# Kernel tuning notes

Measured on AMD Instinct MI355X. Metric: run time of the kernel, lower is better.

The kernel has to match this reference:

```python
import jax, jax.numpy as jnp
import numpy as np

B, T, D, H, O = 64, 512, 512, 2048, 7

def setup_inputs() -> dict:
    key = jax.random.key(0)
    ks = jax.random.split(key, 12)
    s_ih = 1.0 / np.sqrt(H)
    return {
        "x":    jax.random.normal(ks[0], (B, T, D), dtype=jnp.float32),
        # LSTMCell params (PyTorch gate order i,f,g,o stacked along dim 0)
        "W_ih": jax.random.uniform(ks[1], (4 * H, D), jnp.float32, -s_ih, s_ih),
        "b_ih": jax.random.uniform(ks[2], (4 * H,), jnp.float32, -s_ih, s_ih),
        "W_hh": jax.random.uniform(ks[3], (4 * H, H), jnp.float32, -s_ih, s_ih),
        "b_hh": jax.random.uniform(ks[4], (4 * H,), jnp.float32, -s_ih, s_ih),
        # init_h / init_c Linear(D -> H)
        "W_h0": jax.random.normal(ks[5], (H, D), jnp.float32) * np.sqrt(2.0 / D),
        "b_h0": jnp.zeros((H,), jnp.float32),
        "W_c0": jax.random.normal(ks[6], (H, D), jnp.float32) * np.sqrt(2.0 / D),
        "b_c0": jnp.zeros((H,), jnp.float32),
        # fc Linear(H -> O), kaiming init, zero bias
        "W_fc": jax.random.normal(ks[7], (O, H), jnp.float32) * np.sqrt(2.0 / H),
        "b_fc": jnp.zeros((O,), jnp.float32),
    }

def reference(x, W_ih, b_ih, W_hh, b_hh, W_h0, b_h0, W_c0, b_c0, W_fc, b_fc):
    # init hidden state from mean over time (module's init_hidden_state)
    mean_x = x.mean(axis=1)                       # [B, D]
    h0 = mean_x @ W_h0.T + b_h0                   # [B, H]
    c0 = mean_x @ W_c0.T + b_c0                   # [B, H]

    def step(carry, xt):
        h, c = carry
        gates = xt @ W_ih.T + b_ih + h @ W_hh.T + b_hh   # [B, 4H]
        i, f, g, o = jnp.split(gates, 4, axis=1)
        i = jax.nn.sigmoid(i)
        f = jax.nn.sigmoid(f)
        g = jnp.tanh(g)
        o = jax.nn.sigmoid(o)
        c = f * c + i * g
        h = o * jnp.tanh(c)
        return (h, c), h

    xs = jnp.swapaxes(x, 0, 1)                    # [T, B, D]
    _, hs = jax.lax.scan(step, (h0, c0), xs)      # hs: [T, B, H]
    # dropout(p=0.5) is identity in eval mode; fc per timestep
    poses = jnp.einsum('tbh,oh->bto', hs, W_fc) + b_fc   # [B, T, O]
    return poses
```

## Files before the change

kernel.cpp:

```cpp
#include <hip/hip_runtime.h>
#include <hip/hip_cooperative_groups.h>

namespace cg = cooperative_groups;

#define Bb 64
#define Tt 512
#define Dd 512
#define Hh 2048
#define Oo 7
#define NKT 80
#define NWG 256
#define NTHR 512
#define SP 36
#define HSTEP 131072
#define XSTEP 32768

typedef short bf16x8 __attribute__((ext_vector_type(8)));
typedef float f32x4 __attribute__((ext_vector_type(4)));

__device__ __forceinline__ unsigned short f2bf(float f) {
  unsigned u = __float_as_uint(f);
  return (unsigned short)((u + 0x7FFFu + ((u >> 16) & 1u)) >> 16);
}
__device__ __forceinline__ float bf2f(unsigned short s) {
  return __uint_as_float(((unsigned)s) << 16);
}
__device__ __forceinline__ float sigm(float x) { return 1.0f / (1.0f + __expf(-x)); }
__device__ __forceinline__ float tanh_(float x) {
  x = fminf(15.0f, fmaxf(-15.0f, x));
  float e = __expf(2.0f * x);
  return (e - 1.0f) / (e + 1.0f);
}

__global__ void __launch_bounds__(NTHR, 2) lstm_fused(
    const float* __restrict__ x,
    const float* __restrict__ W_ih, const float* __restrict__ b_ih,
    const float* __restrict__ W_hh, const float* __restrict__ b_hh,
    const float* __restrict__ W_h0, const float* __restrict__ b_h0,
    const float* __restrict__ W_c0, const float* __restrict__ b_c0,
    const float* __restrict__ W_fc, const float* __restrict__ b_fc,
    float* __restrict__ out,
    short* __restrict__ Wbf,
    unsigned short* __restrict__ Hbuf,
    float* __restrict__ cbuf,
    float* __restrict__ meanx,
    float* __restrict__ bsum,
    unsigned short* __restrict__ xbf,
    unsigned* __restrict__ flags)
{
  const int wg = blockIdx.x, tid = threadIdx.x;
  const int gtid = wg * NTHR + tid;
  cg::grid_group grid = cg::this_grid();
  __shared__ float smem[8 * 64 * SP];

  {
    int b = wg >> 2;
    int d = ((wg & 3) << 7) + (tid & 127);
    int th = tid >> 7;
    const float* xp = x + (size_t)b * Tt * Dd + d;
    float s = 0.f;
    for (int t = th * 128; t < th * 128 + 128; ++t) s += xp[(size_t)t * Dd];
    smem[tid] = s;
    __syncthreads();
    if (tid < 128) {
      float tot = smem[tid] + smem[tid + 128] + smem[tid + 256] + smem[tid + 384];
      meanx[b * Dd + ((wg & 3) << 7) + tid] = tot * (1.0f / Tt);
    }
    __syncthreads();
  }

  {
    const int NSLOT = (8192 * 2560) / 8;
    for (int slot = gtid; slot < NSLOT; slot += NWG * NTHR) {
      int lane = slot & 63;
      int fr = slot >> 6;
      int kt = fr % 80;
      int ntw = fr / 80;
      int nl = ((ntw & 1) << 4) + (lane & 15);
      int w = ntw >> 1;
      int row = ((nl >> 3) << 11) + (w << 3) + (nl & 7);
      int kb = (kt << 5) + ((lane >> 4) << 3);
      const float* src = (kb < 512) ? (W_ih + (size_t)row * 512 + kb)
                                    : (W_hh + (size_t)row * 2048 + (kb - 512));
      float4 u0 = *reinterpret_cast<const float4*>(src);
      float4 u1 = *reinterpret_cast<const float4*>(src + 4);
      bf16x8 v;
      v[0] = (short)f2bf(u0.x); v[1] = (short)f2bf(u0.y);
      v[2] = (short)f2bf(u0.z); v[3] = (short)f2bf(u0.w);
      v[4] = (short)f2bf(u1.x); v[5] = (short)f2bf(u1.y);
      v[6] = (short)f2bf(u1.z); v[7] = (short)f2bf(u1.w);
      *reinterpret_cast<bf16x8*>(Wbf + (size_t)slot * 8) = v;
    }
    const int NX = (Bb * Tt * Dd) / 8;
    for (int s = gtid; s < NX; s += NWG * NTHR) {
      int q  = s & 3;
      int b  = (s >> 2) & 63;
      int kt = (s >> 8) & 15;
      int t  = s >> 12;
      const float* p = x + (size_t)b * (Tt * Dd) + (size_t)t * Dd + (kt << 5) + (q << 3);
      float4 u0 = *reinterpret_cast<const float4*>(p);
      float4 u1 = *reinterpret_cast<const float4*>(p + 4);
      bf16x8 v;
      v[0] = (short)f2bf(u0.x); v[1] = (short)f2bf(u0.y);
      v[2] = (short)f2bf(u0.z); v[3] = (short)f2bf(u0.w);
      v[4] = (short)f2bf(u1.x); v[5] = (short)f2bf(u1.y);
      v[6] = (short)f2bf(u1.z); v[7] = (short)f2bf(u1.w);
      *reinterpret_cast<bf16x8*>((short*)xbf + (size_t)s * 8) = v;
    }
    if (gtid < NWG)
      __hip_atomic_store(&flags[gtid], 0u, __ATOMIC_RELAXED, __HIP_MEMORY_SCOPE_AGENT);
    if (gtid < 8192) bsum[gtid] = b_ih[gtid] + b_hh[gtid];
  }
  grid.sync();

  {
    for (int q = tid; q < 1024; q += NTHR) {
      int which = q >> 9;
      int b = (q >> 3) & 63;
      int j = q & 7;
      int n = (wg << 3) + j;
      const float* Wr = (which ? W_c0 : W_h0) + (size_t)n * 512;
      const float* mx = meanx + b * 512;
      float acc0 = which ? b_c0[n] : b_h0[n];
      for (int d = 0; d < 512; ++d) acc0 += mx[d] * Wr[d];
      if (which) cbuf[b * Hh + n] = acc0;
      else       Hbuf[((n >> 5) << 11) + (b << 5) + (n & 31)] = f2bf(acc0);
    }
  }
  grid.sync();

  const int wave = tid >> 6, lane = tid & 63;
  const int ml = lane & 15;
  const int kg = lane >> 4;
  const short* wb0 = Wbf + (size_t)(wg * 2) * NKT * 512;
  const short* wb1 = wb0 + (size_t)NKT * 512;

  bf16x8 w0x[2], w0h[8], w1x[2], w1h[8];
#pragma unroll
  for (int i = 0; i < 2; ++i) {
    int kt = (wave << 1) + i;
    w0x[i] = *reinterpret_cast<const bf16x8*>(wb0 + ((size_t)kt << 9) + (lane << 3));
    w1x[i] = *reinterpret_cast<const bf16x8*>(wb1 + ((size_t)kt << 9) + (lane << 3));
  }
#pragma unroll
  for (int i = 0; i < 8; ++i) {
    int kt = 16 + (wave << 3) + i;
    w0h[i] = *reinterpret_cast<const bf16x8*>(wb0 + ((size_t)kt << 9) + (lane << 3));
    w1h[i] = *reinterpret_cast<const bf16x8*>(wb1 + ((size_t)kt << 9) + (lane << 3));
  }

  const int cb = tid >> 3, cj = tid & 7;
  const int cn = (wg << 3) + cj;
  float cv = cbuf[cb * Hh + cn];
  const float bi = bsum[cn],        bfs = bsum[2048 + cn];
  const float bg = bsum[4096 + cn], bo = bsum[6144 + cn];

  f32x4 acc[4][2];
#pragma unroll
  for (int mt = 0; mt < 4; ++mt) {
    acc[mt][0] = (f32x4){0.f, 0.f, 0.f, 0.f};
    acc[mt][1] = (f32x4){0.f, 0.f, 0.f, 0.f};
  }

  auto xpart = [&](int tx) {
#pragma unroll
    for (int i = 0; i < 2; ++i) {
      int kt = (wave << 1) + i;
      const unsigned short* xb = xbf + (size_t)tx * XSTEP + ((size_t)kt << 11) + (kg << 3);
      bf16x8 afr[4];
#pragma unroll
      for (int mt = 0; mt < 4; ++mt) {
        int m = (mt << 4) + ml;
        afr[mt] = *reinterpret_cast<const bf16x8*>(xb + (m << 5));
      }
#pragma unroll
      for (int mt = 0; mt < 4; ++mt) {
        acc[mt][0] = __builtin_amdgcn_mfma_f32_16x16x32_bf16(afr[mt], w0x[i], acc[mt][0], 0, 0, 0);
        acc[mt][1] = __builtin_amdgcn_mfma_f32_16x16x32_bf16(afr[mt], w1x[i], acc[mt][1], 0, 0, 0);
      }
    }
  };

  auto waitwave = [&](unsigned tw) {
    const unsigned* fl = flags + ((wave << 5) | (lane & 31));
    while (__hip_atomic_load(fl, __ATOMIC_RELAXED, __HIP_MEMORY_SCOPE_AGENT) < tw)
      __builtin_amdgcn_s_sleep(2);
    asm volatile("" ::: "memory");
  };

  auto waitall = [&](unsigned tw) {
    if (wave == 0) {
      const unsigned* fl = flags + (lane << 2);
      for (;;) {
        unsigned m0 = __hip_atomic_load(&fl[0], __ATOMIC_RELAXED, __HIP_MEMORY_SCOPE_AGENT);
        unsigned m1 = __hip_atomic_load(&fl[1], __ATOMIC_RELAXED, __HIP_MEMORY_SCOPE_AGENT);
        unsigned m2 = __hip_atomic_load(&fl[2], __ATOMIC_RELAXED, __HIP_MEMORY_SCOPE_AGENT);
        unsigned m3 = __hip_atomic_load(&fl[3], __ATOMIC_RELAXED, __HIP_MEMORY_SCOPE_AGENT);
        unsigned mn = min(min(m0, m1), min(m2, m3));
        if (__all(mn >= tw)) break;
        __builtin_amdgcn_s_sleep(2);
      }
    }
    asm volatile("" ::: "memory");
    __syncthreads();
  };

  xpart(0);

  for (int t = 1; t <= Tt; ++t) {
    if (t > 1) waitwave((unsigned)(t - 1));
#pragma unroll
    for (int i = 0; i < 8; ++i) {
      int kth = (wave << 3) + i;
      const unsigned short* hb = Hbuf + (size_t)(t - 1) * HSTEP + ((size_t)kth << 11) + (kg << 3);
      bf16x8 afr[4];
#pragma unroll
      for (int mt = 0; mt < 4; ++mt) {
        int m = (mt << 4) + ml;
        afr[mt] = *reinterpret_cast<const bf16x8*>(hb + (m << 5));
      }
#pragma unroll
      for (int mt = 0; mt < 4; ++mt) {
        acc[mt][0] = __builtin_amdgcn_mfma_f32_16x16x32_bf16(afr[mt], w0h[i], acc[mt][0], 0, 0, 0);
        acc[mt][1] = __builtin_amdgcn_mfma_f32_16x16x32_bf16(afr[mt], w1h[i], acc[mt][1], 0, 0, 0);
      }
    }
#pragma unroll
    for (int mt = 0; mt < 4; ++mt) {
      int r0 = (mt << 4) + (kg << 2);
#pragma unroll
      for (int r = 0; r < 4; ++r) {
        smem[((wave << 6) + r0 + r) * SP + ml] = acc[mt][0][r];
        smem[((wave << 6) + r0 + r) * SP + 16 + ml] = acc[mt][1][r];
      }
    }
    __syncthreads();
    unsigned* hout32 = (unsigned*)(Hbuf + (size_t)t * HSTEP);
    {
      float gi = 0.f, gf_ = 0.f, gg = 0.f, go = 0.f;
#pragma unroll
      for (int w2 = 0; w2 < 8; ++w2) {
        const float* sp = &smem[((w2 << 6) + cb) * SP];
        gi += sp[cj];       gf_ += sp[8 + cj];
        gg += sp[16 + cj];  go += sp[24 + cj];
      }
      gi += bi; gf_ += bfs; gg += bg; go += bo;
      cv = sigm(gf_) * cv + sigm(gi) * tanh_(gg);
      float hv = sigm(go) * tanh_(cv);
      float hv_hi = __shfl_down(hv, 1);
      if (!(tid & 1)) {
        unsigned pk = ((unsigned)f2bf(hv_hi) << 16) | (unsigned)f2bf(hv);
        int soff = ((cn >> 5) << 11) + (cb << 5) + (cn & 31);
        __hip_atomic_store(&hout32[soff >> 1], pk,
                           __ATOMIC_RELAXED, __HIP_MEMORY_SCOPE_AGENT);
      }
    }
    asm volatile("s_waitcnt vmcnt(0)" ::: "memory");
    __syncthreads();
    if (tid == 0)
      __hip_atomic_store(&flags[wg], (unsigned)t,
                         __ATOMIC_RELAXED, __HIP_MEMORY_SCOPE_AGENT);
#pragma unroll
    for (int mt = 0; mt < 4; ++mt) {
      acc[mt][0] = (f32x4){0.f, 0.f, 0.f, 0.f};
      acc[mt][1] = (f32x4){0.f, 0.f, 0.f, 0.f};
    }
    if (t < Tt) xpart(t);
  }

  waitall((unsigned)Tt);

  for (int i = tid; i < Oo * Hh; i += NTHR) smem[i] = W_fc[i];
  __syncthreads();
  if (gtid < Bb * Tt) {
    int b = gtid & 63, tq = gtid >> 6;
    const unsigned short* hrw = Hbuf + (size_t)(tq + 1) * HSTEP + (b << 5);
    float acco[7];
#pragma unroll
    for (int o = 0; o < 7; ++o) acco[o] = b_fc[o];
    for (int k = 0; k < Hh; k += 8) {
      bf16x8 hv = *reinterpret_cast<const bf16x8*>(hrw + ((k >> 5) << 11) + (k & 31));
      float hf[8];
#pragma unroll
      for (int e = 0; e < 8; ++e) hf[e] = bf2f((unsigned short)hv[e]);
#pragma unroll
      for (int o = 0; o < 7; ++o) {
        const float* wr = &smem[o * Hh + k];
        float s = 0.f;
#pragma unroll
        for (int e = 0; e < 8; ++e) s += hf[e] * wr[e];
        acco[o] += s;
      }
    }
    float* op = out + ((size_t)b * Tt + tq) * Oo;
#pragma unroll
    for (int o = 0; o < 7; ++o) op[o] = acco[o];
  }
}

extern "C" void kernel_launch(void* const* d_in, const int* in_sizes, int n_in,
                              void* d_out, int out_size, void* d_ws, size_t ws_size,
                              hipStream_t stream) {
  (void)in_sizes; (void)n_in;
  const float* x    = (const float*)d_in[0];
  const float* W_ih = (const float*)d_in[1];
  const float* b_ih = (const float*)d_in[2];
  const float* W_hh = (const float*)d_in[3];
  const float* b_hh = (const float*)d_in[4];
  const float* W_h0 = (const float*)d_in[5];
  const float* b_h0 = (const float*)d_in[6];
  const float* W_c0 = (const float*)d_in[7];
  const float* b_c0 = (const float*)d_in[8];
  const float* W_fc = (const float*)d_in[9];
  const float* b_fc = (const float*)d_in[10];
  float* out = (float*)d_out;

  char* ws = (char*)d_ws;
  size_t off = 0;
  short* Wbf = (short*)(ws + off);            off += (size_t)8192 * 2560 * 2;
  unsigned short* Hbuf = (unsigned short*)(ws + off); off += (size_t)513 * 64 * 2048 * 2;
  float* cbuf = (float*)(ws + off);           off += (size_t)64 * 2048 * 4;
  float* meanx = (float*)(ws + off);          off += (size_t)64 * 512 * 4;
  float* bsum = (float*)(ws + off);           off += (size_t)8192 * 4;
  unsigned short* xbf = (unsigned short*)(ws + off); off += (size_t)64 * 512 * 512 * 2;
  unsigned* flags = (unsigned*)(ws + off);    off += (size_t)NWG * 4;

  if (ws_size < off) {
    hipMemsetAsync(d_out, 0, (size_t)out_size * 4, stream);
    return;
  }

  void* args[] = {&x, &W_ih, &b_ih, &W_hh, &b_hh, &W_h0, &b_h0, &W_c0, &b_c0,
                  &W_fc, &b_fc, &out, &Wbf, &Hbuf, &cbuf, &meanx, &bsum, &xbf, &flags};
  hipLaunchCooperativeKernel((void*)lstm_fused, dim3(NWG), dim3(NTHR), args, 0, stream);
}
```

Measured before the change: 3.925 ms.

## Split batch across workgroup halves and stream weights from global per step

Repartitions the persistent LSTM so each workgroup owns 32 batch rows and 16 hidden units (64 gate columns) instead of all 64 rows and 8 hidden units. Waits now depend only on the 128 workgroups in the same batch half, which shrinks the set of producers each step has to wait for. Weights are no longer kept in registers and are reloaded from global memory (L2) every timestep, raising per-step load traffic. The reduction buffer layout and the h packing shuffle are adjusted to match.

```diff
diff --git a/kernel.cpp b/kernel.cpp
--- a/kernel.cpp
+++ b/kernel.cpp
@@ -11,9 +11,10 @@
 #define NKT 80
 #define NWG 256
 #define NTHR 512
-#define SP 36
+#define SP 70
 #define HSTEP 131072
 #define XSTEP 32768
+#define WSLC (NKT * 512)
 
 typedef short bf16x8 __attribute__((ext_vector_type(8)));
 typedef float f32x4 __attribute__((ext_vector_type(4)));
@@ -51,7 +52,9 @@
   const int wg = blockIdx.x, tid = threadIdx.x;
   const int gtid = wg * NTHR + tid;
   cg::grid_group grid = cg::this_grid();
-  __shared__ float smem[8 * 64 * SP];
+  __shared__ float smem[256 * SP];
+
+  const int bh = wg >> 7, cgp = wg & 127;
 
   {
     int b = wg >> 2;
@@ -114,17 +117,18 @@
   grid.sync();
 
   {
-    for (int q = tid; q < 1024; q += NTHR) {
-      int which = q >> 9;
-      int b = (q >> 3) & 63;
-      int j = q & 7;
-      int n = (wg << 3) + j;
+    for (int q2 = tid; q2 < 1024; q2 += NTHR) {
+      int which = q2 >> 9;
+      int r = q2 & 511;
+      int lb2 = r >> 4, j = r & 15;
+      int b = (bh << 5) + lb2;
+      int n = (cgp << 4) + j;
       const float* Wr = (which ? W_c0 : W_h0) + (size_t)n * 512;
       const float* mx = meanx + b * 512;
-      float acc0 = which ? b_c0[n] : b_h0[n];
-      for (int d = 0; d < 512; ++d) acc0 += mx[d] * Wr[d];
-      if (which) cbuf[b * Hh + n] = acc0;
-      else       Hbuf[((n >> 5) << 11) + (b << 5) + (n & 31)] = f2bf(acc0);
+      float a0 = which ? b_c0[n] : b_h0[n];
+      for (int d = 0; d < 512; ++d) a0 += mx[d] * Wr[d];
+      if (which) cbuf[b * Hh + n] = a0;
+      else       Hbuf[((n >> 5) << 11) + (b << 5) + (n & 31)] = f2bf(a0);
     }
   }
   grid.sync();
@@ -132,57 +136,44 @@
   const int wave = tid >> 6, lane = tid & 63;
   const int ml = lane & 15;
   const int kg = lane >> 4;
-  const short* wb0 = Wbf + (size_t)(wg * 2) * NKT * 512;
-  const short* wb1 = wb0 + (size_t)NKT * 512;
-
-  bf16x8 w0x[2], w0h[8], w1x[2], w1h[8];
-#pragma unroll
-  for (int i = 0; i < 2; ++i) {
-    int kt = (wave << 1) + i;
-    w0x[i] = *reinterpret_cast<const bf16x8*>(wb0 + ((size_t)kt << 9) + (lane << 3));
-    w1x[i] = *reinterpret_cast<const bf16x8*>(wb1 + ((size_t)kt << 9) + (lane << 3));
-  }
-#pragma unroll
-  for (int i = 0; i < 8; ++i) {
-    int kt = 16 + (wave << 3) + i;
-    w0h[i] = *reinterpret_cast<const bf16x8*>(wb0 + ((size_t)kt << 9) + (lane << 3));
-    w1h[i] = *reinterpret_cast<const bf16x8*>(wb1 + ((size_t)kt << 9) + (lane << 3));
-  }
-
-  const int cb = tid >> 3, cj = tid & 7;
-  const int cn = (wg << 3) + cj;
-  float cv = cbuf[cb * Hh + cn];
+  const short* wbase = Wbf + (size_t)(cgp << 2) * WSLC;
+
+  const int lb = tid & 31, hc = tid >> 5;
+  const int cbn = (bh << 5) + lb;
+  const int cn  = (cgp << 4) + hc;
+  float cv = cbuf[cbn * Hh + cn];
   const float bi = bsum[cn],        bfs = bsum[2048 + cn];
   const float bg = bsum[4096 + cn], bo = bsum[6144 + cn];
 
-  f32x4 acc[4][2];
-#pragma unroll
-  for (int mt = 0; mt < 4; ++mt) {
-    acc[mt][0] = (f32x4){0.f, 0.f, 0.f, 0.f};
-    acc[mt][1] = (f32x4){0.f, 0.f, 0.f, 0.f};
-  }
+  f32x4 acc[2][4];
+#pragma unroll
+  for (int mt = 0; mt < 2; ++mt)
+#pragma unroll
+    for (int q = 0; q < 4; ++q) acc[mt][q] = (f32x4){0.f, 0.f, 0.f, 0.f};
 
   auto xpart = [&](int tx) {
 #pragma unroll
     for (int i = 0; i < 2; ++i) {
       int kt = (wave << 1) + i;
-      const unsigned short* xb = xbf + (size_t)tx * XSTEP + ((size_t)kt << 11) + (kg << 3);
-      bf16x8 afr[4];
-#pragma unroll
-      for (int mt = 0; mt < 4; ++mt) {
-        int m = (mt << 4) + ml;
-        afr[mt] = *reinterpret_cast<const bf16x8*>(xb + (m << 5));
-      }
-#pragma unroll
-      for (int mt = 0; mt < 4; ++mt) {
-        acc[mt][0] = __builtin_amdgcn_mfma_f32_16x16x32_bf16(afr[mt], w0x[i], acc[mt][0], 0, 0, 0);
-        acc[mt][1] = __builtin_amdgcn_mfma_f32_16x16x32_bf16(afr[mt], w1x[i], acc[mt][1], 0, 0, 0);
+      const unsigned short* xb = xbf + (size_t)tx * XSTEP + ((size_t)kt << 11)
+                                     + (bh << 10) + (kg << 3);
+      bf16x8 afr[2];
+#pragma unroll
+      for (int mt = 0; mt < 2; ++mt)
+        afr[mt] = *reinterpret_cast<const bf16x8*>(xb + (((mt << 4) + ml) << 5));
+      const short* wk = wbase + ((size_t)kt << 9) + (lane << 3);
+#pragma unroll
+      for (int q = 0; q < 4; ++q) {
+        bf16x8 bq = *reinterpret_cast<const bf16x8*>(wk + (size_t)q * WSLC);
+#pragma unroll
+        for (int mt = 0; mt < 2; ++mt)
+          acc[mt][q] = __builtin_amdgcn_mfma_f32_16x16x32_bf16(afr[mt], bq, acc[mt][q], 0, 0, 0);
       }
     }
   };
 
   auto waitwave = [&](unsigned tw) {
-    const unsigned* fl = flags + ((wave << 5) | (lane & 31));
+    const unsigned* fl = flags + (bh << 7) + (wave << 4) + (lane & 15);
     while (__hip_atomic_load(fl, __ATOMIC_RELAXED, __HIP_MEMORY_SCOPE_AGENT) < tw)
       __builtin_amdgcn_s_sleep(2);
     asm volatile("" ::: "memory");
@@ -211,27 +202,30 @@
     if (t > 1) waitwave((unsigned)(t - 1));
 #pragma unroll
     for (int i = 0; i < 8; ++i) {
-      int kth = (wave << 3) + i;
-      const unsigned short* hb = Hbuf + (size_t)(t - 1) * HSTEP + ((size_t)kth << 11) + (kg << 3);
-      bf16x8 afr[4];
-#pragma unroll
-      for (int mt = 0; mt < 4; ++mt) {
-        int m = (mt << 4) + ml;
-        afr[mt] = *reinterpret_cast<const bf16x8*>(hb + (m << 5));
-      }
-#pragma unroll
-      for (int mt = 0; mt < 4; ++mt) {
-        acc[mt][0] = __builtin_amdgcn_mfma_f32_16x16x32_bf16(afr[mt], w0h[i], acc[mt][0], 0, 0, 0);
-        acc[mt][1] = __builtin_amdgcn_mfma_f32_16x16x32_bf16(afr[mt], w1h[i], acc[mt][1], 0, 0, 0);
-      }
-    }
-#pragma unroll
-    for (int mt = 0; mt < 4; ++mt) {
-      int r0 = (mt << 4) + (kg << 2);
+      int nb = (wave << 3) + i;
+      const unsigned short* hb = Hbuf + (size_t)(t - 1) * HSTEP + ((size_t)nb << 11)
+                                      + (bh << 10) + (kg << 3);
+      bf16x8 afr[2];
+#pragma unroll
+      for (int mt = 0; mt < 2; ++mt)
+        afr[mt] = *reinterpret_cast<const bf16x8*>(hb + (((mt << 4) + ml) << 5));
+      const short* wk = wbase + ((size_t)(16 + nb) << 9) + (lane << 3);
+#pragma unroll
+      for (int q = 0; q < 4; ++q) {
+        bf16x8 bq = *reinterpret_cast<const bf16x8*>(wk + (size_t)q * WSLC);
+#pragma unroll
+        for (int mt = 0; mt < 2; ++mt)
+          acc[mt][q] = __builtin_amdgcn_mfma_f32_16x16x32_bf16(afr[mt], bq, acc[mt][q], 0, 0, 0);
+      }
+    }
+#pragma unroll
+    for (int mt = 0; mt < 2; ++mt) {
+      int r0 = (wave << 5) + (mt << 4) + (kg << 2);
 #pragma unroll
       for (int r = 0; r < 4; ++r) {
-        smem[((wave << 6) + r0 + r) * SP + ml] = acc[mt][0][r];
-        smem[((wave << 6) + r0 + r) * SP + 16 + ml] = acc[mt][1][r];
+        float* sr = &smem[(r0 + r) * SP];
+#pragma unroll
+        for (int q = 0; q < 4; ++q) sr[(q << 4) + ml] = acc[mt][q][r];
       }
     }
     __syncthreads();
@@ -240,17 +234,16 @@
       float gi = 0.f, gf_ = 0.f, gg = 0.f, go = 0.f;
 #pragma unroll
       for (int w2 = 0; w2 < 8; ++w2) {
-        const float* sp = &smem[((w2 << 6) + cb) * SP];
-        gi += sp[cj];       gf_ += sp[8 + cj];
-        gg += sp[16 + cj];  go += sp[24 + cj];
+        const float* sp = &smem[((w2 << 5) + lb) * SP + ((hc >> 3) << 5) + (hc & 7)];
+        gi += sp[0]; gf_ += sp[8]; gg += sp[16]; go += sp[24];
       }
       gi += bi; gf_ += bfs; gg += bg; go += bo;
       cv = sigm(gf_) * cv + sigm(gi) * tanh_(gg);
       float hv = sigm(go) * tanh_(cv);
-      float hv_hi = __shfl_down(hv, 1);
-      if (!(tid & 1)) {
+      float hv_hi = __shfl_down(hv, 32);
+      if (!((tid >> 5) & 1)) {
         unsigned pk = ((unsigned)f2bf(hv_hi) << 16) | (unsigned)f2bf(hv);
-        int soff = ((cn >> 5) << 11) + (cb << 5) + (cn & 31);
+        int soff = ((cn >> 5) << 11) + (cbn << 5) + (cn & 31);
         __hip_atomic_store(&hout32[soff >> 1], pk,
                            __ATOMIC_RELAXED, __HIP_MEMORY_SCOPE_AGENT);
       }
@@ -261,10 +254,9 @@
       __hip_atomic_store(&flags[wg], (unsigned)t,
                          __ATOMIC_RELAXED, __HIP_MEMORY_SCOPE_AGENT);
 #pragma unroll
-    for (int mt = 0; mt < 4; ++mt) {
-      acc[mt][0] = (f32x4){0.f, 0.f, 0.f, 0.f};
-      acc[mt][1] = (f32x4){0.f, 0.f, 0.f, 0.f};
-    }
+    for (int mt = 0; mt < 2; ++mt)
+#pragma unroll
+      for (int q = 0; q < 4; ++q) acc[mt][q] = (f32x4){0.f, 0.f, 0.f, 0.f};
     if (t < Tt) xpart(t);
   }
 
```

After: 4.917 ms. 1.25x slower.
